# Optimization experiments

Hardware: AMD Instinct MI355X
Metric: run time of the kernel (lower is better)

Reference implementation:

```python
import jax, jax.numpy as jnp
import numpy as np

BLOCK_SIZE = 32
EPS = 1e-6


def setup_inputs() -> dict:
    key = jax.random.key(0)
    k1, k2, k3, k4, k5 = jax.random.split(key, 5)
    B, H, L, D = 2, 16, 4096, 128
    return {
        "query_states": jax.random.normal(k1, (B, H, L, D), dtype=jnp.float32),
        "key_states": jax.random.normal(k2, (B, H, L, D), dtype=jnp.float32),
        "value_states": jax.random.normal(k3, (B, H, L, D), dtype=jnp.float32),
        # learned params; init near torch defaults (ones/zeros) with small noise
        "phi_scale": 1.0 + 0.1 * jax.random.normal(k4, (H, 1, D), dtype=jnp.float32),
        "phi_bias": 0.1 * jax.random.normal(k5, (H, 1, D), dtype=jnp.float32),
    }


def _forward(query_states, key_states, value_states, phi_scale, phi_bias):
    B, H, L, D = query_states.shape
    bs = BLOCK_SIZE
    N = L // bs  # L chosen divisible by block_size (no padding path)

    def feature_map(x):  # x: (B,H,N,bs,D)
        # phi_scale (H,1,D) -> (H,1,1,D) broadcasts over (B,H,N,bs,D)
        y = jax.nn.elu(x * phi_scale[:, None] + phi_bias[:, None]) + 1.0
        return jnp.clip(y, 0.0, 10.0)

    q = query_states.reshape(B, H, N, bs, D)
    k = key_states.reshape(B, H, N, bs, D)
    v = value_states.reshape(B, H, N, bs, D)

    phi_q = feature_map(q)
    phi_k = feature_map(k)

    # move block axis to front for scan: (N,B,H,bs,D)
    pq = jnp.moveaxis(phi_q, 2, 0)
    pk = jnp.moveaxis(phi_k, 2, 0)
    vb = jnp.moveaxis(v, 2, 0)

    S0 = jnp.zeros((B, H, D, D), dtype=jnp.float32)
    Z0 = jnp.zeros((B, H, D), dtype=jnp.float32)

    def step(carry, inp):
        S, Z = carry
        pq_n, pk_n, v_n = inp  # each (B,H,bs,D)
        # block-causal, bidirectional within block: update state BEFORE output
        S = S + jnp.einsum('bhkd,bhke->bhde', pk_n, v_n)
        Z = Z + pk_n.sum(axis=-2)
        num = jnp.einsum('bhqd,bhde->bhqe', pq_n, S)
        den = jnp.maximum(jnp.einsum('bhqd,bhd->bhq', pq_n, Z), EPS)
        return (S, Z), num / den[..., None]

    _, out_blocks = jax.lax.scan(step, (S0, Z0), (pq, pk, vb))  # (N,B,H,bs,D)
    out = jnp.moveaxis(out_blocks, 0, 2).reshape(B, H, L, D)
    return out


def reference(query_states, key_states, value_states, phi_scale, phi_bias):
    return _forward(query_states, key_states, value_states, phi_scale, phi_bias)
```

## Files before the change

### kernel.cpp

```cpp
#include <hip/hip_runtime.h>
#include <stdint.h>

#define BH 32
#define LSEQ 4096
#define DDIM 128
#define CHUNKS 16
#define CHUNK_ROWS 256
#define STATE_SZ (DDIM*DDIM + DDIM)

typedef __attribute__((ext_vector_type(8))) short bf16x8;
typedef __attribute__((ext_vector_type(4))) float f32x4;

__device__ inline uint16_t f2bf(float f) {
    uint32_t x = __builtin_bit_cast(uint32_t, f);
    x += 0x7fffu + ((x >> 16) & 1u);
    return (uint16_t)(x >> 16);
}
__device__ inline uint32_t pack2(float a, float b) {
    return (uint32_t)f2bf(a) | ((uint32_t)f2bf(b) << 16);
}
__device__ inline float phi_f(float x, float s, float b) {
    float y = fmaf(x, s, b);
    float pos = fminf(y + 1.0f, 10.0f);
    float neg = __expf(y);
    return (y > 0.0f) ? pos : neg;
}
__device__ inline void bar_lgkm() {
    asm volatile("s_waitcnt lgkmcnt(0)\n\ts_barrier" ::: "memory");
}

#define SMEM1 67584
__global__ __launch_bounds__(512, 4) void la_state(
    const float* __restrict__ K, const float* __restrict__ V,
    const float* __restrict__ scale, const float* __restrict__ bias,
    float* __restrict__ states)
{
    extern __shared__ char smem[];
    const int tid  = threadIdx.x;
    const int bh   = blockIdx.x >> 4;
    const int ch   = blockIdx.x & 15;
    const int h    = bh & 15;
    const int lane = tid & 63;
    const int wid  = tid >> 6;
    const int i15  = lane & 15;
    const int q4   = lane >> 4;
    const size_t base = (size_t)bh * LSEQ * DDIM;
    const int row0 = ch * CHUNK_ROWS;

    const int d  = tid & 127;
    const int rg = tid >> 7;
    const float sk = scale[h*DDIM + d];
    const float bk = bias [h*DDIM + d];

    f32x4 accS[8];
    #pragma unroll
    for (int mt = 0; mt < 8; ++mt) accS[mt] = (f32x4){0.f,0.f,0.f,0.f};
    float zacc = 0.f;

    float kreg[16], vreg[16];
    auto load_kv = [&](int g) {
        const float* Kc = K + base + (size_t)(row0 + 64*g + 16*rg)*DDIM + d;
        const float* Vc = V + base + (size_t)(row0 + 64*g + 16*rg)*DDIM + d;
        #pragma unroll
        for (int j = 0; j < 16; ++j) {
            kreg[j] = Kc[(size_t)j*DDIM];
            vreg[j] = Vc[(size_t)j*DDIM];
        }
    };
    auto stage = [&](int b) {
        uint32_t wk[8], wv8[8];
        #pragma unroll
        for (int j = 0; j < 8; ++j) {
            float p0 = phi_f(kreg[2*j],   sk, bk);
            float p1 = phi_f(kreg[2*j+1], sk, bk);
            zacc += p0 + p1;
            wk[j]  = pack2(p0, p1);
            wv8[j] = pack2(vreg[2*j], vreg[2*j+1]);
        }
        char* pkb = smem + b*16384;
        char* vtb = smem + 32768 + b*16384;
        const uint32_t lin = (uint32_t)(d*128 + 32*rg);
        const uint32_t swz = (uint32_t)((d & 7) << 4);
        *(uint4*)(pkb + ((lin     ) ^ swz)) = ((const uint4*)wk)[0];
        *(uint4*)(pkb + ((lin + 16) ^ swz)) = ((const uint4*)wk)[1];
        *(uint4*)(vtb + ((lin     ) ^ swz)) = ((const uint4*)wv8)[0];
        *(uint4*)(vtb + ((lin + 16) ^ swz)) = ((const uint4*)wv8)[1];
    };

    load_kv(0);
    stage(0);
    load_kv(1);
    bar_lgkm();

    #pragma unroll
    for (int g = 0; g < 4; ++g) {
        if (g < 3) stage((g+1)&1);
        if (g < 2) load_kv(g+2);
        const char* pkb = smem + (g&1)*16384;
        const char* vtb = smem + 32768 + (g&1)*16384;
        const uint32_t swz = (uint32_t)((i15 & 7) << 4);
        #pragma unroll
        for (int ksl = 0; ksl < 2; ++ksl) {
            bf16x8 bv = *(const bf16x8*)(vtb + (((uint32_t)((16*wid+i15)*128 + 64*ksl + 16*q4)) ^ swz));
            #pragma unroll
            for (int mt = 0; mt < 8; ++mt) {
                bf16x8 av = *(const bf16x8*)(pkb + (((uint32_t)((16*mt+i15)*128 + 64*ksl + 16*q4)) ^ swz));
                accS[mt] = __builtin_amdgcn_mfma_f32_16x16x32_bf16(av, bv, accS[mt], 0, 0, 0);
            }
        }
        bar_lgkm();
    }

    float* Zpart = (float*)(smem + 65536);
    Zpart[rg*128 + d] = zacc;
    float* stb = states + (size_t)(bh*CHUNKS + ch)*STATE_SZ;
    #pragma unroll
    for (int mt = 0; mt < 8; ++mt)
        #pragma unroll
        for (int r = 0; r < 4; ++r)
            stb[(size_t)(16*mt + 4*q4 + r)*DDIM + 16*wid + i15] = accS[mt][r];
    bar_lgkm();
    if (tid < 128)
        stb[DDIM*DDIM + tid] = Zpart[tid] + Zpart[128+tid] + Zpart[256+tid] + Zpart[384+tid];
}

__global__ void la_prefix(float* __restrict__ states) {
    const int bh  = blockIdx.y;
    const int idx = blockIdx.x * 128 + threadIdx.x;
    float* p = states + (size_t)bh * CHUNKS * STATE_SZ + idx;
    float run = 0.f;
    #pragma unroll
    for (int c = 0; c < CHUNKS; ++c) {
        float v = p[(size_t)c * STATE_SZ];
        p[(size_t)c * STATE_SZ] = run;
        run += v;
    }
}

#define SMEM2 119808
__global__ __launch_bounds__(512, 2) void la_fwd(
    const float* __restrict__ Q, const float* __restrict__ K,
    const float* __restrict__ V, const float* __restrict__ scale,
    const float* __restrict__ bias, const float* __restrict__ states,
    float* __restrict__ out)
{
    extern __shared__ char smem[];
    const int tid  = threadIdx.x;
    const int bh   = blockIdx.x >> 4;
    const int ch   = blockIdx.x & 15;
    const int h    = bh & 15;
    const int lane = tid & 63;
    const int wid  = tid >> 6;
    const int i15  = lane & 15;
    const int q4   = lane >> 4;
    const size_t base = (size_t)bh * LSEQ * DDIM;
    const int row0 = ch * CHUNK_ROWS;
    const float* stb = states + (size_t)(bh*CHUNKS + ch)*STATE_SZ;

    const int krow = tid >> 3;
    const int kd8  = (tid & 7) * 16;
    const int ve   = tid & 127;
    const int vrg  = tid >> 7;

    float skr[16], bkr[16];
    #pragma unroll
    for (int u = 0; u < 4; ++u) {
        *(float4*)&skr[4*u] = *(const float4*)(scale + h*DDIM + kd8 + 4*u);
        *(float4*)&bkr[4*u] = *(const float4*)(bias  + h*DDIM + kd8 + 4*u);
    }

    float4 kq[4];
    float  vr[16];
    auto load_kv = [&](int g) {
        const float* Kr = K + base + (size_t)(row0 + 64*g + krow)*DDIM + kd8;
        #pragma unroll
        for (int u = 0; u < 4; ++u) kq[u] = *(const float4*)(Kr + 4*u);
        const float* Vc = V + base + (size_t)(row0 + 64*g + 16*vrg)*DDIM + ve;
        #pragma unroll
        for (int j = 0; j < 16; ++j) vr[j] = Vc[(size_t)j*DDIM];
    };
    auto stage_kv = [&](int b) {
        char* pkb = smem + 32768 + b*32768;
        char* vtb = pkb + 16384;
        uint32_t wk[8];
        #pragma unroll
        for (int u = 0; u < 4; ++u) {
            float x0 = phi_f(kq[u].x, skr[4*u+0], bkr[4*u+0]);
            float x1 = phi_f(kq[u].y, skr[4*u+1], bkr[4*u+1]);
            float x2 = phi_f(kq[u].z, skr[4*u+2], bkr[4*u+2]);
            float x3 = phi_f(kq[u].w, skr[4*u+3], bkr[4*u+3]);
            wk[2*u]   = pack2(x0, x1);
            wk[2*u+1] = pack2(x2, x3);
        }
        uint32_t lin = (uint32_t)(krow*256 + kd8*2);
        uint32_t swz = (uint32_t)((krow & 7) << 4);
        *(uint4*)(pkb + ((lin     ) ^ swz)) = ((const uint4*)wk)[0];
        *(uint4*)(pkb + ((lin + 16) ^ swz)) = ((const uint4*)wk)[1];
        uint32_t wv8[8];
        #pragma unroll
        for (int j = 0; j < 8; ++j) wv8[j] = pack2(vr[2*j], vr[2*j+1]);
        lin = (uint32_t)(ve*128 + 32*vrg);
        swz = (uint32_t)((ve & 7) << 4);
        *(uint4*)(vtb + ((lin     ) ^ swz)) = ((const uint4*)wv8)[0];
        *(uint4*)(vtb + ((lin + 16) ^ swz)) = ((const uint4*)wv8)[1];
    };

    load_kv(0);

    {
        const int se  = tid & 127;
        const int sdg = tid >> 7;
        float sv[32];
        const float* srcp = stb + (size_t)(32*sdg)*DDIM + se;
        #pragma unroll
        for (int k2 = 0; k2 < 32; ++k2) sv[k2] = srcp[(size_t)k2*DDIM];
        uint32_t wbuf[16];
        #pragma unroll
        for (int k2 = 0; k2 < 16; ++k2) wbuf[k2] = pack2(sv[2*k2], sv[2*k2+1]);
        const uint32_t linb = (uint32_t)(se*256 + 64*sdg);
        const uint32_t swz  = (uint32_t)((se & 7) << 4);
        #pragma unroll
        for (int m = 0; m < 4; ++m)
            *(uint4*)(smem + ((linb + 16*m) ^ swz)) = ((const uint4*)wbuf)[m];
    }

    stage_kv(0);
    load_kv(1);

    bf16x8 pq[2][4];
    float dacc0 = 0.f, dacc1 = 0.f;
    #pragma unroll
    for (int ks = 0; ks < 4; ++ks) {
        const float* sp = scale + h*DDIM + 32*ks + 8*q4;
        const float* bp = bias  + h*DDIM + 32*ks + 8*q4;
        const float* zp = stb + DDIM*DDIM + 32*ks + 8*q4;
        float4 s0 = *(const float4*)sp, s1 = *(const float4*)(sp+4);
        float4 b0 = *(const float4*)bp, b1 = *(const float4*)(bp+4);
        float4 z0 = *(const float4*)zp, z1 = *(const float4*)(zp+4);
        #pragma unroll
        for (int qt = 0; qt < 2; ++qt) {
            const float* qp = Q + base + (size_t)(row0 + 32*wid + 16*qt + i15)*DDIM + 32*ks + 8*q4;
            float4 a0 = *(const float4*)qp, a1 = *(const float4*)(qp+4);
            float f0 = phi_f(a0.x, s0.x, b0.x), f1 = phi_f(a0.y, s0.y, b0.y);
            float f2 = phi_f(a0.z, s0.z, b0.z), f3 = phi_f(a0.w, s0.w, b0.w);
            float f4 = phi_f(a1.x, s1.x, b1.x), f5 = phi_f(a1.y, s1.y, b1.y);
            float f6 = phi_f(a1.z, s1.z, b1.z), f7 = phi_f(a1.w, s1.w, b1.w);
            float ds = f0*z0.x + f1*z0.y + f2*z0.z + f3*z0.w
                     + f4*z1.x + f5*z1.y + f6*z1.z + f7*z1.w;
            if (qt == 0) dacc0 += ds; else dacc1 += ds;
            uint4 uu = { pack2(f0,f1), pack2(f2,f3), pack2(f4,f5), pack2(f6,f7) };
            pq[qt][ks] = __builtin_bit_cast(bf16x8, uu);
        }
    }

    bar_lgkm();

    f32x4 acc[2][8];
    #pragma unroll
    for (int qt = 0; qt < 2; ++qt)
        #pragma unroll
        for (int et = 0; et < 8; ++et) acc[qt][et] = (f32x4){0.f,0.f,0.f,0.f};
    {
        const uint32_t swz = (uint32_t)((i15 & 7) << 4);
        #pragma unroll
        for (int ks = 0; ks < 4; ++ks)
            #pragma unroll
            for (int et = 0; et < 8; ++et) {
                bf16x8 sb = *(const bf16x8*)(smem + (((uint32_t)((16*et+i15)*256 + 64*ks + 16*q4)) ^ swz));
                acc[0][et] = __builtin_amdgcn_mfma_f32_16x16x32_bf16(pq[0][ks], sb, acc[0][et], 0, 0, 0);
                acc[1][et] = __builtin_amdgcn_mfma_f32_16x16x32_bf16(pq[1][ks], sb, acc[1][et], 0, 0, 0);
            }
    }

    #pragma unroll
    for (int it = 0; it < 4; ++it) {
        if (it < 3) stage_kv((it+1)&1);
        if (it < 2) load_kv(it+2);
        const char* pkb = smem + 32768 + (it&1)*32768;
        const char* vtb = pkb + 16384;
        const uint32_t swz = (uint32_t)((i15 & 7) << 4);
        #pragma unroll
        for (int tl = 0; tl < 2; ++tl) {
            const int t = 2*it + tl;
            if (t <= wid) {
                f32x4 Aacc[2][2];
                #pragma unroll
                for (int rt = 0; rt < 2; ++rt)
                    #pragma unroll
                    for (int qt = 0; qt < 2; ++qt) Aacc[rt][qt] = (f32x4){0.f,0.f,0.f,0.f};
                #pragma unroll
                for (int ks = 0; ks < 4; ++ks) {
                    bf16x8 ak0 = *(const bf16x8*)(pkb + (((uint32_t)((32*tl      + i15)*256 + 64*ks + 16*q4)) ^ swz));
                    bf16x8 ak1 = *(const bf16x8*)(pkb + (((uint32_t)((32*tl + 16 + i15)*256 + 64*ks + 16*q4)) ^ swz));
                    Aacc[0][0] = __builtin_amdgcn_mfma_f32_16x16x32_bf16(ak0, pq[0][ks], Aacc[0][0], 0, 0, 0);
                    Aacc[0][1] = __builtin_amdgcn_mfma_f32_16x16x32_bf16(ak0, pq[1][ks], Aacc[0][1], 0, 0, 0);
                    Aacc[1][0] = __builtin_amdgcn_mfma_f32_16x16x32_bf16(ak1, pq[0][ks], Aacc[1][0], 0, 0, 0);
                    Aacc[1][1] = __builtin_amdgcn_mfma_f32_16x16x32_bf16(ak1, pq[1][ks], Aacc[1][1], 0, 0, 0);
                }
                dacc0 += Aacc[0][0][0]+Aacc[0][0][1]+Aacc[0][0][2]+Aacc[0][0][3]
                       + Aacc[1][0][0]+Aacc[1][0][1]+Aacc[1][0][2]+Aacc[1][0][3];
                dacc1 += Aacc[0][1][0]+Aacc[0][1][1]+Aacc[0][1][2]+Aacc[0][1][3]
                       + Aacc[1][1][0]+Aacc[1][1][1]+Aacc[1][1][2]+Aacc[1][1][3];
                char* al = smem + 98304 + wid*2560;
                #pragma unroll
                for (int rt = 0; rt < 2; ++rt)
                    #pragma unroll
                    for (int qt = 0; qt < 2; ++qt) {
                        uint2 o;
                        o.x = pack2(Aacc[rt][qt][0], Aacc[rt][qt][1]);
                        o.y = pack2(Aacc[rt][qt][2], Aacc[rt][qt][3]);
                        *(uint2*)(al + (uint32_t)(((16*qt + i15)*40 + 16*rt + 4*q4)*2)) = o;
                    }
                bf16x8 aq0 = *(const bf16x8*)(al + (uint32_t)((      i15*40 + 8*q4)*2));
                bf16x8 aq1 = *(const bf16x8*)(al + (uint32_t)(((16 + i15)*40 + 8*q4)*2));
                #pragma unroll
                for (int et = 0; et < 8; ++et) {
                    bf16x8 bvv = *(const bf16x8*)(vtb + (((uint32_t)((16*et+i15)*128 + 64*tl + 16*q4)) ^ swz));
                    acc[0][et] = __builtin_amdgcn_mfma_f32_16x16x32_bf16(aq0, bvv, acc[0][et], 0, 0, 0);
                    acc[1][et] = __builtin_amdgcn_mfma_f32_16x16x32_bf16(aq1, bvv, acc[1][et], 0, 0, 0);
                }
            }
        }
        bar_lgkm();
    }

    dacc0 += __shfl_xor(dacc0, 16, 64); dacc0 += __shfl_xor(dacc0, 32, 64);
    dacc1 += __shfl_xor(dacc1, 16, 64); dacc1 += __shfl_xor(dacc1, 32, 64);
    float* denl = (float*)(smem + 118784);
    if (q4 == 0) {
        denl[wid*32 + i15]      = dacc0;
        denl[wid*32 + 16 + i15] = dacc1;
    }
    #pragma unroll
    for (int qt = 0; qt < 2; ++qt) {
        float inv[4];
        #pragma unroll
        for (int r = 0; r < 4; ++r)
            inv[r] = 1.0f / fmaxf(denl[wid*32 + 16*qt + 4*q4 + r], 1e-6f);
        #pragma unroll
        for (int et = 0; et < 8; ++et)
            #pragma unroll
            for (int r = 0; r < 4; ++r)
                out[base + (size_t)(row0 + 32*wid + 16*qt + 4*q4 + r)*DDIM + 16*et + i15] =
                    acc[qt][et][r] * inv[r];
    }
}

extern "C" void kernel_launch(void* const* d_in, const int* in_sizes, int n_in,
                              void* d_out, int out_size, void* d_ws, size_t ws_size,
                              hipStream_t stream) {
    const float* Q     = (const float*)d_in[0];
    const float* K     = (const float*)d_in[1];
    const float* V     = (const float*)d_in[2];
    const float* scale = (const float*)d_in[3];
    const float* bias  = (const float*)d_in[4];
    float* out    = (float*)d_out;
    float* states = (float*)d_ws;

    static bool s_attr = false;
    if (!s_attr) {
        hipFuncSetAttribute(reinterpret_cast<const void*>(la_state),
                            hipFuncAttributeMaxDynamicSharedMemorySize, SMEM1);
        hipFuncSetAttribute(reinterpret_cast<const void*>(la_fwd),
                            hipFuncAttributeMaxDynamicSharedMemorySize, SMEM2);
        s_attr = true;
    }

    hipLaunchKernelGGL(la_state, dim3(BH*CHUNKS), dim3(512), SMEM1, stream,
                       K, V, scale, bias, states);
    hipLaunchKernelGGL(la_prefix, dim3(129, BH), dim3(128), 0, stream, states);
    hipLaunchKernelGGL(la_fwd, dim3(BH*CHUNKS), dim3(512), SMEM2, stream,
                       Q, K, V, scale, bias, states, out);
}
```

Before: 306.5 us.

## Shrink la_fwd LDS footprint and balance causal work across waves

Restructures the forward kernel to stream K/V in 32-row tiles instead of 64, shrinking shared memory from about 117KB to 70KB and raising launch bounds to 4 blocks per CU. Each wave now owns a pair of 16-row query tiles (wid and 15-wid), so per-wave causal intra-chunk work is balanced. The S0 staging area is reused as per-wave scratch, and scale/bias are kept in LDS instead of registers. This adds twice as many barrier iterations and halves the work per stage, which could expose more latency.

```diff
diff --git a/kernel.cpp b/kernel.cpp
--- a/kernel.cpp
+++ b/kernel.cpp
@@ -137,14 +137,20 @@
     }
 }
 
-#define SMEM2 119808
-__global__ __launch_bounds__(512, 2) void la_fwd(
+#define SMEM2 71680
+__global__ __launch_bounds__(512, 4) void la_fwd(
     const float* __restrict__ Q, const float* __restrict__ K,
     const float* __restrict__ V, const float* __restrict__ scale,
     const float* __restrict__ bias, const float* __restrict__ states,
     float* __restrict__ out)
 {
     extern __shared__ char smem[];
+    char* S0T  = smem;
+    char* pkB  = smem + 32768;
+    char* vtB  = smem + 49152;
+    float* sbL  = (float*)(smem + 69632);
+    float* denl = (float*)(smem + 70656);
+
     const int tid  = threadIdx.x;
     const int bh   = blockIdx.x >> 4;
     const int ch   = blockIdx.x & 15;
@@ -157,78 +163,68 @@
     const int row0 = ch * CHUNK_ROWS;
     const float* stb = states + (size_t)(bh*CHUNKS + ch)*STATE_SZ;
 
-    const int krow = tid >> 3;
-    const int kd8  = (tid & 7) * 16;
+    const int krow = tid >> 4;
+    const int kc8  = (tid & 15) * 8;
     const int ve   = tid & 127;
     const int vrg  = tid >> 7;
 
-    float skr[16], bkr[16];
-    #pragma unroll
-    for (int u = 0; u < 4; ++u) {
-        *(float4*)&skr[4*u] = *(const float4*)(scale + h*DDIM + kd8 + 4*u);
-        *(float4*)&bkr[4*u] = *(const float4*)(bias  + h*DDIM + kd8 + 4*u);
-    }
-
-    float4 kq[4];
-    float  vr[16];
+    const int qa0 = wid, qa1 = 15 - wid;
+    const int jmax0 = qa0 >> 1, jmax1 = qa1 >> 1;
+
+    float4 kq[2];
+    float  vr[8];
     auto load_kv = [&](int g) {
-        const float* Kr = K + base + (size_t)(row0 + 64*g + krow)*DDIM + kd8;
-        #pragma unroll
-        for (int u = 0; u < 4; ++u) kq[u] = *(const float4*)(Kr + 4*u);
-        const float* Vc = V + base + (size_t)(row0 + 64*g + 16*vrg)*DDIM + ve;
-        #pragma unroll
-        for (int j = 0; j < 16; ++j) vr[j] = Vc[(size_t)j*DDIM];
+        const float* Kr = K + base + (size_t)(row0 + 32*g + krow)*DDIM + kc8;
+        kq[0] = *(const float4*)(Kr);
+        kq[1] = *(const float4*)(Kr + 4);
+        const float* Vc = V + base + (size_t)(row0 + 32*g + 8*vrg)*DDIM + ve;
+        #pragma unroll
+        for (int j = 0; j < 8; ++j) vr[j] = Vc[(size_t)j*DDIM];
     };
     auto stage_kv = [&](int b) {
-        char* pkb = smem + 32768 + b*32768;
-        char* vtb = pkb + 16384;
-        uint32_t wk[8];
-        #pragma unroll
-        for (int u = 0; u < 4; ++u) {
-            float x0 = phi_f(kq[u].x, skr[4*u+0], bkr[4*u+0]);
-            float x1 = phi_f(kq[u].y, skr[4*u+1], bkr[4*u+1]);
-            float x2 = phi_f(kq[u].z, skr[4*u+2], bkr[4*u+2]);
-            float x3 = phi_f(kq[u].w, skr[4*u+3], bkr[4*u+3]);
-            wk[2*u]   = pack2(x0, x1);
-            wk[2*u+1] = pack2(x2, x3);
-        }
-        uint32_t lin = (uint32_t)(krow*256 + kd8*2);
-        uint32_t swz = (uint32_t)((krow & 7) << 4);
-        *(uint4*)(pkb + ((lin     ) ^ swz)) = ((const uint4*)wk)[0];
-        *(uint4*)(pkb + ((lin + 16) ^ swz)) = ((const uint4*)wk)[1];
-        uint32_t wv8[8];
-        #pragma unroll
-        for (int j = 0; j < 8; ++j) wv8[j] = pack2(vr[2*j], vr[2*j+1]);
-        lin = (uint32_t)(ve*128 + 32*vrg);
-        swz = (uint32_t)((ve & 7) << 4);
-        *(uint4*)(vtb + ((lin     ) ^ swz)) = ((const uint4*)wv8)[0];
-        *(uint4*)(vtb + ((lin + 16) ^ swz)) = ((const uint4*)wv8)[1];
+        float4 s0 = *(const float4*)&sbL[kc8];
+        float4 s1 = *(const float4*)&sbL[kc8 + 4];
+        float4 b0 = *(const float4*)&sbL[128 + kc8];
+        float4 b1 = *(const float4*)&sbL[128 + kc8 + 4];
+        uint32_t wk[4];
+        wk[0] = pack2(phi_f(kq[0].x, s0.x, b0.x), phi_f(kq[0].y, s0.y, b0.y));
+        wk[1] = pack2(phi_f(kq[0].z, s0.z, b0.z), phi_f(kq[0].w, s0.w, b0.w));
+        wk[2] = pack2(phi_f(kq[1].x, s1.x, b1.x), phi_f(kq[1].y, s1.y, b1.y));
+        wk[3] = pack2(phi_f(kq[1].z, s1.z, b1.z), phi_f(kq[1].w, s1.w, b1.w));
+        const uint32_t lin = (uint32_t)(krow*256 + kc8*2);
+        const uint32_t swz = (uint32_t)((krow & 7) << 4);
+        *(uint4*)(pkB + b*8192 + (lin ^ swz)) = *(const uint4*)wk;
+        uint32_t wv8[4];
+        #pragma unroll
+        for (int j = 0; j < 4; ++j) wv8[j] = pack2(vr[2*j], vr[2*j+1]);
+        *(uint4*)(vtB + b*10240 + (uint32_t)(ve*80 + vrg*16)) = *(const uint4*)wv8;
     };
 
     load_kv(0);
+
+    if (tid < 256) sbL[tid] = (tid < 128) ? scale[h*DDIM + tid] : bias[h*DDIM + tid - 128];
 
     {
         const int se  = tid & 127;
         const int sdg = tid >> 7;
-        float sv[32];
-        const float* srcp = stb + (size_t)(32*sdg)*DDIM + se;
-        #pragma unroll
-        for (int k2 = 0; k2 < 32; ++k2) sv[k2] = srcp[(size_t)k2*DDIM];
-        uint32_t wbuf[16];
-        #pragma unroll
-        for (int k2 = 0; k2 < 16; ++k2) wbuf[k2] = pack2(sv[2*k2], sv[2*k2+1]);
-        const uint32_t linb = (uint32_t)(se*256 + 64*sdg);
-        const uint32_t swz  = (uint32_t)((se & 7) << 4);
-        #pragma unroll
-        for (int m = 0; m < 4; ++m)
-            *(uint4*)(smem + ((linb + 16*m) ^ swz)) = ((const uint4*)wbuf)[m];
-    }
-
-    stage_kv(0);
-    load_kv(1);
+        const uint32_t swz = (uint32_t)((se & 7) << 4);
+        #pragma unroll
+        for (int pass = 0; pass < 2; ++pass) {
+            float sv[16];
+            const float* sp = stb + (size_t)(32*sdg + 16*pass)*DDIM + se;
+            #pragma unroll
+            for (int k2 = 0; k2 < 16; ++k2) sv[k2] = sp[(size_t)k2*DDIM];
+            uint32_t wbuf[8];
+            #pragma unroll
+            for (int k2 = 0; k2 < 8; ++k2) wbuf[k2] = pack2(sv[2*k2], sv[2*k2+1]);
+            const uint32_t linb = (uint32_t)(se*256 + (32*sdg + 16*pass)*2);
+            *(uint4*)(S0T + ((linb     ) ^ swz)) = ((const uint4*)wbuf)[0];
+            *(uint4*)(S0T + ((linb + 16) ^ swz)) = ((const uint4*)wbuf)[1];
+        }
+    }
 
     bf16x8 pq[2][4];
-    float dacc0 = 0.f, dacc1 = 0.f;
+    float dden0 = 0.f, dden1 = 0.f;
     #pragma unroll
     for (int ks = 0; ks < 4; ++ks) {
         const float* sp = scale + h*DDIM + 32*ks + 8*q4;
@@ -238,8 +234,9 @@
         float4 b0 = *(const float4*)bp, b1 = *(const float4*)(bp+4);
         float4 z0 = *(const float4*)zp, z1 = *(const float4*)(zp+4);
         #pragma unroll
-        for (int qt = 0; qt < 2; ++qt) {
-            const float* qp = Q + base + (size_t)(row0 + 32*wid + 16*qt + i15)*DDIM + 32*ks + 8*q4;
+        for (int tl = 0; tl < 2; ++tl) {
+            const int a = tl ? qa1 : qa0;
+            const float* qp = Q + base + (size_t)(row0 + 16*a + i15)*DDIM + 32*ks + 8*q4;
             float4 a0 = *(const float4*)qp, a1 = *(const float4*)(qp+4);
             float f0 = phi_f(a0.x, s0.x, b0.x), f1 = phi_f(a0.y, s0.y, b0.y);
             float f2 = phi_f(a0.z, s0.z, b0.z), f3 = phi_f(a0.w, s0.w, b0.w);
@@ -247,102 +244,104 @@
             float f6 = phi_f(a1.z, s1.z, b1.z), f7 = phi_f(a1.w, s1.w, b1.w);
             float ds = f0*z0.x + f1*z0.y + f2*z0.z + f3*z0.w
                      + f4*z1.x + f5*z1.y + f6*z1.z + f7*z1.w;
-            if (qt == 0) dacc0 += ds; else dacc1 += ds;
+            if (tl == 0) dden0 += ds; else dden1 += ds;
             uint4 uu = { pack2(f0,f1), pack2(f2,f3), pack2(f4,f5), pack2(f6,f7) };
-            pq[qt][ks] = __builtin_bit_cast(bf16x8, uu);
-        }
-    }
-
+            pq[tl][ks] = __builtin_bit_cast(bf16x8, uu);
+        }
+    }
+
+    stage_kv(0);
+    load_kv(1);
     bar_lgkm();
 
     f32x4 acc[2][8];
     #pragma unroll
-    for (int qt = 0; qt < 2; ++qt)
-        #pragma unroll
-        for (int et = 0; et < 8; ++et) acc[qt][et] = (f32x4){0.f,0.f,0.f,0.f};
+    for (int tl = 0; tl < 2; ++tl)
+        #pragma unroll
+        for (int et = 0; et < 8; ++et) acc[tl][et] = (f32x4){0.f,0.f,0.f,0.f};
     {
         const uint32_t swz = (uint32_t)((i15 & 7) << 4);
         #pragma unroll
         for (int ks = 0; ks < 4; ++ks)
             #pragma unroll
             for (int et = 0; et < 8; ++et) {
-                bf16x8 sb = *(const bf16x8*)(smem + (((uint32_t)((16*et+i15)*256 + 64*ks + 16*q4)) ^ swz));
+                bf16x8 sb = *(const bf16x8*)(S0T + (((uint32_t)((16*et+i15)*256 + (32*ks + 8*q4)*2)) ^ swz));
                 acc[0][et] = __builtin_amdgcn_mfma_f32_16x16x32_bf16(pq[0][ks], sb, acc[0][et], 0, 0, 0);
                 acc[1][et] = __builtin_amdgcn_mfma_f32_16x16x32_bf16(pq[1][ks], sb, acc[1][et], 0, 0, 0);
             }
     }
-
-    #pragma unroll
-    for (int it = 0; it < 4; ++it) {
-        if (it < 3) stage_kv((it+1)&1);
-        if (it < 2) load_kv(it+2);
-        const char* pkb = smem + 32768 + (it&1)*32768;
-        const char* vtb = pkb + 16384;
-        const uint32_t swz = (uint32_t)((i15 & 7) << 4);
+    stage_kv(1);
+    load_kv(2);
+    bar_lgkm();
+
+    char* Ascr0 = S0T + wid*2560;
+    char* Ascr1 = Ascr0 + 1280;
+    const uint32_t swzf = (uint32_t)((i15 & 7) << 4);
+
+    #pragma unroll
+    for (int t = 0; t < 8; ++t) {
+        if (t >= 1) {
+            if (t + 1 <= 7) stage_kv((t+1)&1);
+            if (t + 2 <= 7) load_kv(t+2);
+        }
+        const char* pk = pkB + (t&1)*8192;
+        const char* vt = vtB + (t&1)*10240;
         #pragma unroll
         for (int tl = 0; tl < 2; ++tl) {
-            const int t = 2*it + tl;
-            if (t <= wid) {
-                f32x4 Aacc[2][2];
-                #pragma unroll
-                for (int rt = 0; rt < 2; ++rt)
-                    #pragma unroll
-                    for (int qt = 0; qt < 2; ++qt) Aacc[rt][qt] = (f32x4){0.f,0.f,0.f,0.f};
+            const int jm = tl ? jmax1 : jmax0;
+            if (t <= jm) {
+                char* As = tl ? Ascr1 : Ascr0;
+                f32x4 Aacc[2];
+                Aacc[0] = (f32x4){0.f,0.f,0.f,0.f};
+                Aacc[1] = (f32x4){0.f,0.f,0.f,0.f};
                 #pragma unroll
                 for (int ks = 0; ks < 4; ++ks) {
-                    bf16x8 ak0 = *(const bf16x8*)(pkb + (((uint32_t)((32*tl      + i15)*256 + 64*ks + 16*q4)) ^ swz));
-                    bf16x8 ak1 = *(const bf16x8*)(pkb + (((uint32_t)((32*tl + 16 + i15)*256 + 64*ks + 16*q4)) ^ swz));
-                    Aacc[0][0] = __builtin_amdgcn_mfma_f32_16x16x32_bf16(ak0, pq[0][ks], Aacc[0][0], 0, 0, 0);
-                    Aacc[0][1] = __builtin_amdgcn_mfma_f32_16x16x32_bf16(ak0, pq[1][ks], Aacc[0][1], 0, 0, 0);
-                    Aacc[1][0] = __builtin_amdgcn_mfma_f32_16x16x32_bf16(ak1, pq[0][ks], Aacc[1][0], 0, 0, 0);
-                    Aacc[1][1] = __builtin_amdgcn_mfma_f32_16x16x32_bf16(ak1, pq[1][ks], Aacc[1][1], 0, 0, 0);
+                    bf16x8 ak0 = *(const bf16x8*)(pk + (((uint32_t)((     i15)*256 + (32*ks + 8*q4)*2)) ^ swzf));
+                    bf16x8 ak1 = *(const bf16x8*)(pk + (((uint32_t)((16 + i15)*256 + (32*ks + 8*q4)*2)) ^ swzf));
+                    bf16x8 pqv = tl ? pq[1][ks] : pq[0][ks];
+                    Aacc[0] = __builtin_amdgcn_mfma_f32_16x16x32_bf16(ak0, pqv, Aacc[0], 0, 0, 0);
+                    Aacc[1] = __builtin_amdgcn_mfma_f32_16x16x32_bf16(ak1, pqv, Aacc[1], 0, 0, 0);
                 }
-                dacc0 += Aacc[0][0][0]+Aacc[0][0][1]+Aacc[0][0][2]+Aacc[0][0][3]
-                       + Aacc[1][0][0]+Aacc[1][0][1]+Aacc[1][0][2]+Aacc[1][0][3];
-                dacc1 += Aacc[0][1][0]+Aacc[0][1][1]+Aacc[0][1][2]+Aacc[0][1][3]
-                       + Aacc[1][1][0]+Aacc[1][1][1]+Aacc[1][1][2]+Aacc[1][1][3];
-                char* al = smem + 98304 + wid*2560;
+                float dsum = Aacc[0][0]+Aacc[0][1]+Aacc[0][2]+Aacc[0][3]
+                           + Aacc[1][0]+Aacc[1][1]+Aacc[1][2]+Aacc[1][3];
+                if (tl == 0) dden0 += dsum; else dden1 += dsum;
                 #pragma unroll
-                for (int rt = 0; rt < 2; ++rt)
-                    #pragma unroll
-                    for (int qt = 0; qt < 2; ++qt) {
-                        uint2 o;
-                        o.x = pack2(Aacc[rt][qt][0], Aacc[rt][qt][1]);
-                        o.y = pack2(Aacc[rt][qt][2], Aacc[rt][qt][3]);
-                        *(uint2*)(al + (uint32_t)(((16*qt + i15)*40 + 16*rt + 4*q4)*2)) = o;
-                    }
-                bf16x8 aq0 = *(const bf16x8*)(al + (uint32_t)((      i15*40 + 8*q4)*2));
-                bf16x8 aq1 = *(const bf16x8*)(al + (uint32_t)(((16 + i15)*40 + 8*q4)*2));
+                for (int sub = 0; sub < 2; ++sub) {
+                    uint2 o;
+                    o.x = pack2(Aacc[sub][0], Aacc[sub][1]);
+                    o.y = pack2(Aacc[sub][2], Aacc[sub][3]);
+                    *(uint2*)(As + (uint32_t)((i15*40 + 16*sub + 4*q4)*2)) = o;
+                }
+                bf16x8 aq = *(const bf16x8*)(As + (uint32_t)((i15*40 + 8*q4)*2));
                 #pragma unroll
                 for (int et = 0; et < 8; ++et) {
-                    bf16x8 bvv = *(const bf16x8*)(vtb + (((uint32_t)((16*et+i15)*128 + 64*tl + 16*q4)) ^ swz));
-                    acc[0][et] = __builtin_amdgcn_mfma_f32_16x16x32_bf16(aq0, bvv, acc[0][et], 0, 0, 0);
-                    acc[1][et] = __builtin_amdgcn_mfma_f32_16x16x32_bf16(aq1, bvv, acc[1][et], 0, 0, 0);
+                    bf16x8 bv = *(const bf16x8*)(vt + (uint32_t)((16*et+i15)*80 + q4*16));
+                    acc[tl][et] = __builtin_amdgcn_mfma_f32_16x16x32_bf16(aq, bv, acc[tl][et], 0, 0, 0);
                 }
             }
         }
         bar_lgkm();
     }
 
-    dacc0 += __shfl_xor(dacc0, 16, 64); dacc0 += __shfl_xor(dacc0, 32, 64);
-    dacc1 += __shfl_xor(dacc1, 16, 64); dacc1 += __shfl_xor(dacc1, 32, 64);
-    float* denl = (float*)(smem + 118784);
+    dden0 += __shfl_xor(dden0, 16, 64); dden0 += __shfl_xor(dden0, 32, 64);
+    dden1 += __shfl_xor(dden1, 16, 64); dden1 += __shfl_xor(dden1, 32, 64);
     if (q4 == 0) {
-        denl[wid*32 + i15]      = dacc0;
-        denl[wid*32 + 16 + i15] = dacc1;
-    }
-    #pragma unroll
-    for (int qt = 0; qt < 2; ++qt) {
+        denl[wid*32 + i15]      = dden0;
+        denl[wid*32 + 16 + i15] = dden1;
+    }
+    #pragma unroll
+    for (int tl = 0; tl < 2; ++tl) {
+        const int a = tl ? qa1 : qa0;
         float inv[4];
         #pragma unroll
         for (int r = 0; r < 4; ++r)
-            inv[r] = 1.0f / fmaxf(denl[wid*32 + 16*qt + 4*q4 + r], 1e-6f);
+            inv[r] = 1.0f / fmaxf(denl[wid*32 + 16*tl + 4*q4 + r], 1e-6f);
         #pragma unroll
         for (int et = 0; et < 8; ++et)
             #pragma unroll
             for (int r = 0; r < 4; ++r)
-                out[base + (size_t)(row0 + 32*wid + 16*qt + 4*q4 + r)*DDIM + 16*et + i15] =
-                    acc[qt][et][r] * inv[r];
+                out[base + (size_t)(row0 + 16*a + 4*q4 + r)*DDIM + 16*et + i15] =
+                    acc[tl][et][r] * inv[r];
     }
 }
 
```

Result: slower. 377.5 us (+23.2%).
